# Performance work log

Hardware: AMD Instinct MI355X
Metric: run time of the kernel (lower is better)

Reference implementation:

```python
import jax, jax.numpy as jnp
import numpy as np

N = 1_048_576
D_IN = 64
D_H = 64
S = 65_536
LN_EPS = 1e-5


def setup_inputs() -> dict:
    key = jax.random.key(0)
    k_x, k_i, k_w, k_b, k_g, k_be = jax.random.split(key, 6)
    X = jax.random.normal(k_x, (N, D_IN), dtype=jnp.float32)
    i = jax.random.randint(k_i, (N,), 0, S, dtype=jnp.int64)
    # Linear(input, hidden) params (torch default init scale ~ 1/sqrt(fan_in))
    W = jax.random.normal(k_w, (D_IN, D_H), dtype=jnp.float32) / np.sqrt(D_IN)
    b = jax.random.normal(k_b, (D_H,), dtype=jnp.float32) * 0.01
    # LayerNorm affine params
    gamma = jnp.ones((D_H,), dtype=jnp.float32)
    beta = jnp.zeros((D_H,), dtype=jnp.float32)
    return {"X": X, "i": i, "W": W, "b": b, "gamma": gamma, "beta": beta,
            "num_segments": S}


def reference(X, i, W, b, gamma, beta, num_segments):
    # fX = ReLU(LayerNorm(Linear(X)))
    h = X @ W + b                               # [N, D_H]
    mu = jnp.mean(h, axis=-1, keepdims=True)
    var = jnp.mean(jnp.square(h - mu), axis=-1, keepdims=True)
    hn = (h - mu) * jax.lax.rsqrt(var + LN_EPS)
    fX = jax.nn.relu(hn * gamma + beta)         # [N, D_H]
    # scatter_max over segments, then gather back per row
    SfX = jax.ops.segment_max(fX, i, num_segments=num_segments)  # [S, D_H]
    return jnp.concatenate([fX, SfX[i]], axis=1)                 # [N, 2*D_H]
```

## Files before the change

### kernel.cpp

```cpp
#include <hip/hip_runtime.h>
#include <hip/hip_bf16.h>

#define N_ROWS 1048576
#define S_SEG  65536
#define LN_EPS 1e-5f

typedef __attribute__((ext_vector_type(8))) short bf16x8;
typedef __attribute__((ext_vector_type(4))) float f32x4;

__device__ __forceinline__ unsigned short f2bf(float x) {
    unsigned u = __float_as_uint(x);
    unsigned r = (u + 0x7FFFu + ((u >> 16) & 1u)) >> 16;
    return (unsigned short)r;
}
__device__ __forceinline__ float bf2f(unsigned short h) {
    return __uint_as_float(((unsigned)h) << 16);
}

__global__ void fused_fwd(const float* __restrict__ X,
                          const int*   __restrict__ idx,
                          const float* __restrict__ W,
                          const float* __restrict__ b,
                          const float* __restrict__ gamma,
                          const float* __restrict__ beta,
                          float* __restrict__ out,
                          int*   __restrict__ sfx)
{
    const int lane = threadIdx.x & 63;
    const int wave = threadIdx.x >> 6;
    const int cl   = lane & 15;
    const int g    = lane >> 4;
    const int ko   = g * 8;

    bf16x8 bhi[4][2], blo[4][2];
    #pragma unroll
    for (int jt = 0; jt < 4; ++jt) {
        #pragma unroll
        for (int s = 0; s < 2; ++s) {
            #pragma unroll
            for (int e = 0; e < 8; ++e) {
                float w = W[(size_t)(s*32 + ko + e) * 64 + jt*16 + cl];
                unsigned short h = f2bf(w);
                unsigned short l = f2bf(w - bf2f(h));
                bhi[jt][s][e] = (short)h;
                blo[jt][s][e] = (short)l;
            }
        }
    }
    float bias[4], gam[4], bet[4];
    #pragma unroll
    for (int jt = 0; jt < 4; ++jt) {
        bias[jt] = b[jt*16 + cl];
        gam[jt]  = gamma[jt*16 + cl];
        bet[jt]  = beta[jt*16 + cl];
    }

    const int nChunks = N_ROWS / 64;
    for (int c = blockIdx.x; c < nChunks; c += gridDim.x) {
        const int r0 = c * 64 + wave * 16;

        int segs[4];
        #pragma unroll
        for (int r = 0; r < 4; ++r)
            segs[r] = idx[r0 + g*4 + r];
        int tcur[4][4];
        #pragma unroll
        for (int r = 0; r < 4; ++r) {
            const int* srow = sfx + (size_t)segs[r] * 64;
            #pragma unroll
            for (int jt = 0; jt < 4; ++jt)
                tcur[r][jt] = srow[jt*16 + cl];
        }

        bf16x8 ahi[2], alo[2];
        const float* xrow = X + (size_t)(r0 + cl) * 64;
        #pragma unroll
        for (int s = 0; s < 2; ++s) {
            f32x4 a0 = __builtin_nontemporal_load((const f32x4*)(xrow + s*32 + ko));
            f32x4 a1 = __builtin_nontemporal_load((const f32x4*)(xrow + s*32 + ko + 4));
            #pragma unroll
            for (int e = 0; e < 4; ++e) {
                unsigned short h0 = f2bf(a0[e]);
                ahi[s][e]   = (short)h0;
                alo[s][e]   = (short)f2bf(a0[e] - bf2f(h0));
                unsigned short h1 = f2bf(a1[e]);
                ahi[s][4+e] = (short)h1;
                alo[s][4+e] = (short)f2bf(a1[e] - bf2f(h1));
            }
        }

        f32x4 acc[4] = {f32x4{0,0,0,0}, f32x4{0,0,0,0}, f32x4{0,0,0,0}, f32x4{0,0,0,0}};
        #pragma unroll
        for (int jt = 0; jt < 4; ++jt) {
            #pragma unroll
            for (int s = 0; s < 2; ++s) {
                acc[jt] = __builtin_amdgcn_mfma_f32_16x16x32_bf16(ahi[s], bhi[jt][s], acc[jt], 0, 0, 0);
                acc[jt] = __builtin_amdgcn_mfma_f32_16x16x32_bf16(ahi[s], blo[jt][s], acc[jt], 0, 0, 0);
                acc[jt] = __builtin_amdgcn_mfma_f32_16x16x32_bf16(alo[s], bhi[jt][s], acc[jt], 0, 0, 0);
            }
        }

        #pragma unroll
        for (int jt = 0; jt < 4; ++jt)
            #pragma unroll
            for (int r = 0; r < 4; ++r)
                acc[jt][r] += bias[jt];

        #pragma unroll
        for (int r = 0; r < 4; ++r) {
            float s1 = acc[0][r] + acc[1][r] + acc[2][r] + acc[3][r];
            float s2 = acc[0][r]*acc[0][r] + acc[1][r]*acc[1][r]
                     + acc[2][r]*acc[2][r] + acc[3][r]*acc[3][r];
            #pragma unroll
            for (int m = 1; m < 16; m <<= 1) {
                s1 += __shfl_xor(s1, m, 64);
                s2 += __shfl_xor(s2, m, 64);
            }
            float mu  = s1 * (1.0f/64.0f);
            float var = s2 * (1.0f/64.0f) - mu*mu;
            float rs  = rsqrtf(var + LN_EPS);

            const int row = r0 + g*4 + r;
            float* orow = out + (size_t)row * 128;
            int*   srow = sfx + (size_t)segs[r] * 64;
            #pragma unroll
            for (int jt = 0; jt < 4; ++jt) {
                float y = (acc[jt][r] - mu) * rs * gam[jt] + bet[jt];
                y = fmaxf(y, 0.0f);
                __builtin_nontemporal_store(y, orow + jt*16 + cl);
                const int yi = __float_as_int(y);
                if (yi > tcur[r][jt])
                    atomicMax(srow + jt*16 + cl, yi);
            }
        }
    }
}

__global__ void gather_k(const int* __restrict__ idx,
                         const float* __restrict__ sfx,
                         float* __restrict__ out)
{
    const int total = N_ROWS * 16;
    for (int t = blockIdx.x * blockDim.x + threadIdx.x; t < total;
         t += gridDim.x * blockDim.x) {
        const int n = t >> 4;
        const int q = t & 15;
        const int seg = idx[n];
        f32x4 v = *(const f32x4*)(sfx + (size_t)seg * 64 + q * 4);
        __builtin_nontemporal_store(v, (f32x4*)(out + (size_t)n * 128 + 64 + q * 4));
    }
}

extern "C" void kernel_launch(void* const* d_in, const int* in_sizes, int n_in,
                              void* d_out, int out_size, void* d_ws, size_t ws_size,
                              hipStream_t stream) {
    const float* X     = (const float*)d_in[0];
    const int*   idx   = (const int*)  d_in[1];
    const float* W     = (const float*)d_in[2];
    const float* b     = (const float*)d_in[3];
    const float* gamma = (const float*)d_in[4];
    const float* beta  = (const float*)d_in[5];
    float* out = (float*)d_out;
    int*   sfx = (int*)d_ws;

    fused_fwd<<<2048, 256, 0, stream>>>(X, idx, W, b, gamma, beta, out, sfx);
    gather_k<<<4096, 256, 0, stream>>>(idx, (const float*)sfx, out);
}
```

Measured before the change: 239.2 us.

## Drop split-bf16 GEMM to single bf16 pass and prefetch next X chunk

Result: faster. 220.2 us (median of 3 runs) (-7.9%).

```diff
diff --git a/kernel.cpp b/kernel.cpp
--- a/kernel.cpp
+++ b/kernel.cpp
@@ -13,18 +13,16 @@
     unsigned r = (u + 0x7FFFu + ((u >> 16) & 1u)) >> 16;
     return (unsigned short)r;
 }
-__device__ __forceinline__ float bf2f(unsigned short h) {
-    return __uint_as_float(((unsigned)h) << 16);
-}
 
-__global__ void fused_fwd(const float* __restrict__ X,
-                          const int*   __restrict__ idx,
-                          const float* __restrict__ W,
-                          const float* __restrict__ b,
-                          const float* __restrict__ gamma,
-                          const float* __restrict__ beta,
-                          float* __restrict__ out,
-                          int*   __restrict__ sfx)
+__global__ __launch_bounds__(256, 4)
+void fused_fwd(const float* __restrict__ X,
+               const int*   __restrict__ idx,
+               const float* __restrict__ W,
+               const float* __restrict__ b,
+               const float* __restrict__ gamma,
+               const float* __restrict__ beta,
+               float* __restrict__ out,
+               int*   __restrict__ sfx)
 {
     const int lane = threadIdx.x & 63;
     const int wave = threadIdx.x >> 6;
@@ -32,21 +30,15 @@
     const int g    = lane >> 4;
     const int ko   = g * 8;
 
-    bf16x8 bhi[4][2], blo[4][2];
+    bf16x8 bhi[4][2];
     #pragma unroll
-    for (int jt = 0; jt < 4; ++jt) {
+    for (int jt = 0; jt < 4; ++jt)
         #pragma unroll
-        for (int s = 0; s < 2; ++s) {
+        for (int s = 0; s < 2; ++s)
             #pragma unroll
-            for (int e = 0; e < 8; ++e) {
-                float w = W[(size_t)(s*32 + ko + e) * 64 + jt*16 + cl];
-                unsigned short h = f2bf(w);
-                unsigned short l = f2bf(w - bf2f(h));
-                bhi[jt][s][e] = (short)h;
-                blo[jt][s][e] = (short)l;
-            }
-        }
-    }
+            for (int e = 0; e < 8; ++e)
+                bhi[jt][s][e] = (short)f2bf(W[(size_t)(s*32 + ko + e) * 64 + jt*16 + cl]);
+
     float bias[4], gam[4], bet[4];
     #pragma unroll
     for (int jt = 0; jt < 4; ++jt) {
@@ -55,14 +47,27 @@
         bet[jt]  = beta[jt*16 + cl];
     }
 
+    const int G = gridDim.x;
     const int nChunks = N_ROWS / 64;
-    for (int c = blockIdx.x; c < nChunks; c += gridDim.x) {
-        const int r0 = c * 64 + wave * 16;
+    int c = blockIdx.x;
 
-        int segs[4];
-        #pragma unroll
-        for (int r = 0; r < 4; ++r)
-            segs[r] = idx[r0 + g*4 + r];
+    f32x4 xb0, xb1, xb2, xb3;
+    {
+        const float* xr = X + (size_t)(c*64 + wave*16 + cl) * 64 + ko;
+        xb0 = __builtin_nontemporal_load((const f32x4*)(xr));
+        xb1 = __builtin_nontemporal_load((const f32x4*)(xr + 4));
+        xb2 = __builtin_nontemporal_load((const f32x4*)(xr + 32));
+        xb3 = __builtin_nontemporal_load((const f32x4*)(xr + 36));
+    }
+    int segs[4];
+    #pragma unroll
+    for (int r = 0; r < 4; ++r)
+        segs[r] = idx[c*64 + wave*16 + g*4 + r];
+
+    while (true) {
+        const int r0 = c*64 + wave*16;
+        const int cn = c + G;
+
         int tcur[4][4];
         #pragma unroll
         for (int r = 0; r < 4; ++r) {
@@ -72,34 +77,33 @@
                 tcur[r][jt] = srow[jt*16 + cl];
         }
 
-        bf16x8 ahi[2], alo[2];
-        const float* xrow = X + (size_t)(r0 + cl) * 64;
+        bf16x8 a0, a1;
         #pragma unroll
-        for (int s = 0; s < 2; ++s) {
-            f32x4 a0 = __builtin_nontemporal_load((const f32x4*)(xrow + s*32 + ko));
-            f32x4 a1 = __builtin_nontemporal_load((const f32x4*)(xrow + s*32 + ko + 4));
+        for (int e = 0; e < 4; ++e) {
+            a0[e]   = (short)f2bf(xb0[e]);
+            a0[4+e] = (short)f2bf(xb1[e]);
+            a1[e]   = (short)f2bf(xb2[e]);
+            a1[4+e] = (short)f2bf(xb3[e]);
+        }
+
+        int segs_n[4];
+        if (cn < nChunks) {
+            const float* xr = X + (size_t)(cn*64 + wave*16 + cl) * 64 + ko;
+            xb0 = __builtin_nontemporal_load((const f32x4*)(xr));
+            xb1 = __builtin_nontemporal_load((const f32x4*)(xr + 4));
+            xb2 = __builtin_nontemporal_load((const f32x4*)(xr + 32));
+            xb3 = __builtin_nontemporal_load((const f32x4*)(xr + 36));
             #pragma unroll
-            for (int e = 0; e < 4; ++e) {
-                unsigned short h0 = f2bf(a0[e]);
-                ahi[s][e]   = (short)h0;
-                alo[s][e]   = (short)f2bf(a0[e] - bf2f(h0));
-                unsigned short h1 = f2bf(a1[e]);
-                ahi[s][4+e] = (short)h1;
-                alo[s][4+e] = (short)f2bf(a1[e] - bf2f(h1));
-            }
+            for (int r = 0; r < 4; ++r)
+                segs_n[r] = idx[cn*64 + wave*16 + g*4 + r];
         }
 
         f32x4 acc[4] = {f32x4{0,0,0,0}, f32x4{0,0,0,0}, f32x4{0,0,0,0}, f32x4{0,0,0,0}};
         #pragma unroll
         for (int jt = 0; jt < 4; ++jt) {
-            #pragma unroll
-            for (int s = 0; s < 2; ++s) {
-                acc[jt] = __builtin_amdgcn_mfma_f32_16x16x32_bf16(ahi[s], bhi[jt][s], acc[jt], 0, 0, 0);
-                acc[jt] = __builtin_amdgcn_mfma_f32_16x16x32_bf16(ahi[s], blo[jt][s], acc[jt], 0, 0, 0);
-                acc[jt] = __builtin_amdgcn_mfma_f32_16x16x32_bf16(alo[s], bhi[jt][s], acc[jt], 0, 0, 0);
-            }
+            acc[jt] = __builtin_amdgcn_mfma_f32_16x16x32_bf16(a0, bhi[jt][0], acc[jt], 0, 0, 0);
+            acc[jt] = __builtin_amdgcn_mfma_f32_16x16x32_bf16(a1, bhi[jt][1], acc[jt], 0, 0, 0);
         }
-
         #pragma unroll
         for (int jt = 0; jt < 4; ++jt)
             #pragma unroll
@@ -133,6 +137,11 @@
                     atomicMax(srow + jt*16 + cl, yi);
             }
         }
+
+        if (cn >= nChunks) break;
+        c = cn;
+        #pragma unroll
+        for (int r = 0; r < 4; ++r) segs[r] = segs_n[r];
     }
 }
 
```
